# Kernel optimization log

Measured on AMD Instinct MI355X. Metric: run time of the kernel, lower is better.

The kernel has to match this reference:

```python
import jax, jax.numpy as jnp
import numpy as np

B, T, DIM = 2, 1024, 4096
H, Hk, D = 32, 8, 128
NREP = H // Hk
SCALE = 1.0 / np.sqrt(D)
LAMBDA_INIT = 0.8 - 0.6 * np.exp(-0.3 * 0)  # layer_idx=0 -> 0.2
EPS = 1e-6


def setup_inputs() -> dict:
    key = jax.random.key(0)
    ks = jax.random.split(key, 12)
    x = jax.random.normal(ks[0], (B, T, DIM), dtype=jnp.float32)
    cos = jax.random.uniform(ks[1], (T, D // 2), dtype=jnp.float32)
    sin = jax.random.uniform(ks[2], (T, D // 2), dtype=jnp.float32)
    wq = jax.random.normal(ks[3], (DIM, 2 * H * D), dtype=jnp.float32) * 0.02
    wk = jax.random.normal(ks[4], (DIM, 2 * Hk * D), dtype=jnp.float32) * 0.02
    wv = jax.random.normal(ks[5], (DIM, Hk * D), dtype=jnp.float32) * 0.02
    wo = jax.random.normal(ks[6], (H * D, DIM), dtype=jnp.float32) * 0.02
    lambda_q1 = jax.random.normal(ks[7], (H, D), dtype=jnp.float32) * 0.1
    lambda_k1 = jax.random.normal(ks[8], (H, D), dtype=jnp.float32) * 0.1
    lambda_q2 = jax.random.normal(ks[9], (H, D), dtype=jnp.float32) * 0.1
    lambda_k2 = jax.random.normal(ks[10], (H, D), dtype=jnp.float32) * 0.1
    subln_w = jnp.ones((D,), dtype=jnp.float32)
    return {"x": x, "cos": cos, "sin": sin, "wq": wq, "wk": wk, "wv": wv,
            "wo": wo, "lambda_q1": lambda_q1, "lambda_k1": lambda_k1,
            "lambda_q2": lambda_q2, "lambda_k2": lambda_k2, "subln_w": subln_w}


def _rope(xh, cos, sin):
    # xh: [B, h, T, D]; cos/sin: [T, D/2]
    x1, x2 = xh[..., : D // 2], xh[..., D // 2:]
    c = cos[None, None, :, :]
    s = sin[None, None, :, :]
    return jnp.concatenate([x1 * c - x2 * s, x2 * c + x1 * s], axis=-1)


def _causal_attn(q, k, v):
    # q,k,v: [B, H, T, D]
    s = jnp.einsum("bhqd,bhkd->bhqk", q, k) * SCALE
    causal = jnp.tril(jnp.ones((T, T), dtype=bool))
    s = jnp.where(causal[None, None], s, jnp.finfo(s.dtype).min)
    p = jax.nn.softmax(s, axis=-1)
    return jnp.einsum("bhqk,bhkd->bhqd", p, v)


def reference(x, cos, sin, wq, wk, wv, wo, lambda_q1, lambda_k1, lambda_q2, lambda_k2, subln_w):
    q_full = (x @ wq).reshape(B, T, 2 * H, D).transpose(0, 2, 1, 3)   # [B,2H,T,D]
    k_full = (x @ wk).reshape(B, T, 2 * Hk, D).transpose(0, 2, 1, 3)  # [B,2Hk,T,D]
    v = (x @ wv).reshape(B, T, Hk, D).transpose(0, 2, 1, 3)           # [B,Hk,T,D]

    q1, q2 = q_full[:, :H], q_full[:, H:]
    k1, k2 = k_full[:, :Hk], k_full[:, Hk:]

    q1 = _rope(q1, cos, sin)
    q2 = _rope(q2, cos, sin)
    k1 = _rope(k1, cos, sin)
    k2 = _rope(k2, cos, sin)

    def expand_kv(kv):  # [B,Hk,T,D] -> [B,H,T,D] (GQA repeat)
        return jnp.repeat(kv, NREP, axis=1)

    k1e, k2e, ve = expand_kv(k1), expand_kv(k2), expand_kv(v)

    a1 = _causal_attn(q1, k1e, ve)
    a2 = _causal_attn(q2, k2e, ve)

    lam = (jnp.exp(jnp.sum(lambda_q1 * lambda_k1, axis=-1))
           - jnp.exp(jnp.sum(lambda_q2 * lambda_k2, axis=-1))
           + LAMBDA_INIT)  # [H]
    diff = a1 - lam[None, :, None, None] * a2  # [B,H,T,D]

    # per-head-dim RMSNorm (subln)
    rms = jax.lax.rsqrt(jnp.mean(diff * diff, axis=-1, keepdims=True) + EPS)
    diff = diff * rms * subln_w

    out = diff.transpose(0, 2, 1, 3).reshape(B, T, H * D)
    return out @ wo
```

## Files before the change

kernel.cpp:

```cpp
#include <hip/hip_runtime.h>
#include <hip/hip_bf16.h>
#include <stdint.h>

typedef unsigned short u16;
typedef unsigned int u32;
typedef short bf16x8 __attribute__((ext_vector_type(8)));
typedef float f32x4 __attribute__((ext_vector_type(4)));

#define SCALE_F 0.088388347648318447f
#define LAMBDA_INIT_F 0.2f

__device__ __forceinline__ u16 f2bf(float f) {
  union { float f; u32 u; } v; v.f = f;
  u32 r = v.u + 0x7fffu + ((v.u >> 16) & 1u);
  return (u16)(r >> 16);
}
__device__ __forceinline__ float bf2f(u16 u) {
  union { u32 u; float f; } v; v.u = ((u32)u) << 16;
  return v.f;
}

typedef __attribute__((address_space(1))) void gvoid_t;
typedef __attribute__((address_space(3))) void lvoid_t;
__device__ __forceinline__ void gload16(const void* g, void* l) {
  __builtin_amdgcn_global_load_lds((gvoid_t*)g, (lvoid_t*)l, 16, 0, 0);
}

__global__ void cast_f32_bf16(const float4* __restrict__ in, uint2* __restrict__ out, int n4) {
  int i = blockIdx.x * 256 + threadIdx.x;
  if (i >= n4) return;
  float4 v = in[i];
  uint2 o;
  o.x = (u32)f2bf(v.x) | ((u32)f2bf(v.y) << 16);
  o.y = (u32)f2bf(v.z) | ((u32)f2bf(v.w) << 16);
  out[i] = o;
}

__global__ void trans_cast(const float* __restrict__ in, u16* __restrict__ out, int K, int N) {
  __shared__ float tile[64][33];
  int kt = blockIdx.y * 64, nt = blockIdx.x * 32;
  int x = threadIdx.x, y = threadIdx.y;
  #pragma unroll
  for (int j = 0; j < 8; ++j)
    tile[y + j * 8][x] = in[(size_t)(kt + y + j * 8) * N + nt + x];
  __syncthreads();
  #pragma unroll
  for (int j = 0; j < 4; ++j) {
    int n = y * 4 + j;
    u32 pk = (u32)f2bf(tile[2 * x][n]) | ((u32)f2bf(tile[2 * x + 1][n]) << 16);
    *(u32*)&out[(size_t)(nt + n) * K + kt + 2 * x] = pk;
  }
}

#define SQA(buf, t) { \
  gload16(Aq + (size_t)(t) * 32, (buf) + qdst); \
  gload16(Aq + (size_t)64 * K + (size_t)(t) * 32, (buf) + 2048 + qdst); }
#define SQB(buf, t) { \
  gload16(Bq + (size_t)(t) * 32, (buf) + qdst); \
  gload16(Bq + (size_t)64 * K + (size_t)(t) * 32, (buf) + 2048 + qdst); \
  gload16(Bq + (size_t)128 * K + (size_t)(t) * 32, (buf) + 4096 + qdst); \
  gload16(Bq + (size_t)192 * K + (size_t)(t) * 32, (buf) + 6144 + qdst); }
#define QMFMA16(O) { \
  acc[O+0][0] = __builtin_amdgcn_mfma_f32_16x16x32_bf16(a0, b0, acc[O+0][0], 0, 0, 0); \
  acc[O+0][1] = __builtin_amdgcn_mfma_f32_16x16x32_bf16(a0, b1, acc[O+0][1], 0, 0, 0); \
  acc[O+0][2] = __builtin_amdgcn_mfma_f32_16x16x32_bf16(a0, b2, acc[O+0][2], 0, 0, 0); \
  acc[O+0][3] = __builtin_amdgcn_mfma_f32_16x16x32_bf16(a0, b3, acc[O+0][3], 0, 0, 0); \
  acc[O+1][0] = __builtin_amdgcn_mfma_f32_16x16x32_bf16(a1, b0, acc[O+1][0], 0, 0, 0); \
  acc[O+1][1] = __builtin_amdgcn_mfma_f32_16x16x32_bf16(a1, b1, acc[O+1][1], 0, 0, 0); \
  acc[O+1][2] = __builtin_amdgcn_mfma_f32_16x16x32_bf16(a1, b2, acc[O+1][2], 0, 0, 0); \
  acc[O+1][3] = __builtin_amdgcn_mfma_f32_16x16x32_bf16(a1, b3, acc[O+1][3], 0, 0, 0); \
  acc[O+2][0] = __builtin_amdgcn_mfma_f32_16x16x32_bf16(a2, b0, acc[O+2][0], 0, 0, 0); \
  acc[O+2][1] = __builtin_amdgcn_mfma_f32_16x16x32_bf16(a2, b1, acc[O+2][1], 0, 0, 0); \
  acc[O+2][2] = __builtin_amdgcn_mfma_f32_16x16x32_bf16(a2, b2, acc[O+2][2], 0, 0, 0); \
  acc[O+2][3] = __builtin_amdgcn_mfma_f32_16x16x32_bf16(a2, b3, acc[O+2][3], 0, 0, 0); \
  acc[O+3][0] = __builtin_amdgcn_mfma_f32_16x16x32_bf16(a3, b0, acc[O+3][0], 0, 0, 0); \
  acc[O+3][1] = __builtin_amdgcn_mfma_f32_16x16x32_bf16(a3, b1, acc[O+3][1], 0, 0, 0); \
  acc[O+3][2] = __builtin_amdgcn_mfma_f32_16x16x32_bf16(a3, b2, acc[O+3][2], 0, 0, 0); \
  acc[O+3][3] = __builtin_amdgcn_mfma_f32_16x16x32_bf16(a3, b3, acc[O+3][3], 0, 0, 0); }

__global__ __launch_bounds__(256, 2) void gemmW(const u16* __restrict__ A,
                                                const u16* __restrict__ Bt,
                                                u16* __restrict__ C,
                                                int M, int N, int K, int TN) {
  extern __shared__ u16 lds[];
  const int tid = threadIdx.x;
  const int lane = tid & 63;
  const int wn = tid >> 6;
  const int ln = lane & 15, gr = lane >> 4;
  const int NT = K >> 5;

  const int bid = blockIdx.x;
  const int bn = (bid % TN) * 256;
  const int bm = (bid / TN) * 128;

  const int sch = (tid & 3) ^ ((tid >> 3) & 3);
  const u16* Aq = A + (size_t)(bm + (tid >> 2)) * K + sch * 8;
  const u16* Bq = Bt + (size_t)(bn + (tid >> 2)) * K + sch * 8;
  const int qdst = tid * 8;

  const int cfo = (gr ^ ((ln >> 1) & 3)) * 8;
  const int ab = ln * 32 + cfo;
  const int bb = wn * 2048 + ln * 32 + cfo;

  f32x4 acc[8][4] = {};
  bf16x8 a0, a1, a2, a3, b0, b1, b2, b3;

  SQA(lds, 0);
  SQB(lds + 12288, 0);
  SQA(lds + 4096, 1);
  SQB(lds + 20480, 1);
  asm volatile("s_waitcnt vmcnt(6)" ::: "memory");
  __builtin_amdgcn_s_barrier();

  int tm3 = 0;
  for (int t = 0; t < NT; ++t) {
    const u16* Ac = lds + tm3 * 4096;
    const u16* Bc = lds + 12288 + tm3 * 8192;
    int tn3 = tm3 + 2; if (tn3 >= 3) tn3 -= 3;
    u16* An = lds + tn3 * 4096;
    u16* Bn = lds + 12288 + tn3 * 8192;

    a0 = *(const bf16x8*)&Ac[ab];
    a1 = *(const bf16x8*)&Ac[ab + 512];
    a2 = *(const bf16x8*)&Ac[ab + 1024];
    a3 = *(const bf16x8*)&Ac[ab + 1536];
    b0 = *(const bf16x8*)&Bc[bb];
    b1 = *(const bf16x8*)&Bc[bb + 512];
    b2 = *(const bf16x8*)&Bc[bb + 1024];
    b3 = *(const bf16x8*)&Bc[bb + 1536];
    if (t + 2 < NT) SQA(An, t + 2);
    __builtin_amdgcn_s_barrier();
    __builtin_amdgcn_s_setprio(1);
    QMFMA16(0);
    __builtin_amdgcn_s_setprio(0);
    __builtin_amdgcn_s_barrier();

    a0 = *(const bf16x8*)&Ac[ab + 2048];
    a1 = *(const bf16x8*)&Ac[ab + 2560];
    a2 = *(const bf16x8*)&Ac[ab + 3072];
    a3 = *(const bf16x8*)&Ac[ab + 3584];
    if (t + 2 < NT) {
      SQB(Bn, t + 2);
      asm volatile("s_waitcnt vmcnt(6)" ::: "memory");
    } else {
      asm volatile("s_waitcnt vmcnt(0)" ::: "memory");
    }
    __builtin_amdgcn_s_barrier();
    __builtin_amdgcn_s_setprio(1);
    QMFMA16(4);
    __builtin_amdgcn_s_setprio(0);
    __builtin_amdgcn_s_barrier();

    tm3 = (tm3 + 1 == 3) ? 0 : tm3 + 1;
  }

  #pragma unroll
  for (int mf = 0; mf < 8; ++mf) {
    #pragma unroll
    for (int j = 0; j < 4; ++j) {
      int r = bm + mf * 16 + gr * 4 + j;
      #pragma unroll
      for (int nf = 0; nf < 4; ++nf) {
        int c = bn + wn * 64 + nf * 16 + ln;
        C[(size_t)r * N + c] = f2bf(acc[mf][nf][j]);
      }
    }
  }
}

#define STA(buf, t) { \
  gload16(Ab + (size_t)(t) * 64, (buf) + dsloc); \
  gload16(Ab + (size_t)32 * K + (size_t)(t) * 64, (buf) + 2048 + dsloc); \
  gload16(Ab + (size_t)64 * K + (size_t)(t) * 64, (buf) + 4096 + dsloc); \
  gload16(Ab + (size_t)96 * K + (size_t)(t) * 64, (buf) + 6144 + dsloc); }
#define STB(buf, t) { \
  gload16(Bb + (size_t)(t) * 64, (buf) + dsloc); \
  gload16(Bb + (size_t)32 * K + (size_t)(t) * 64, (buf) + 2048 + dsloc); \
  gload16(Bb + (size_t)64 * K + (size_t)(t) * 64, (buf) + 4096 + dsloc); \
  gload16(Bb + (size_t)96 * K + (size_t)(t) * 64, (buf) + 6144 + dsloc); }
#define MFMA16 { \
  acc[0][0] = __builtin_amdgcn_mfma_f32_16x16x32_bf16(a0, b0, acc[0][0], 0, 0, 0); \
  acc[0][1] = __builtin_amdgcn_mfma_f32_16x16x32_bf16(a0, b1, acc[0][1], 0, 0, 0); \
  acc[0][2] = __builtin_amdgcn_mfma_f32_16x16x32_bf16(a0, b2, acc[0][2], 0, 0, 0); \
  acc[0][3] = __builtin_amdgcn_mfma_f32_16x16x32_bf16(a0, b3, acc[0][3], 0, 0, 0); \
  acc[1][0] = __builtin_amdgcn_mfma_f32_16x16x32_bf16(a1, b0, acc[1][0], 0, 0, 0); \
  acc[1][1] = __builtin_amdgcn_mfma_f32_16x16x32_bf16(a1, b1, acc[1][1], 0, 0, 0); \
  acc[1][2] = __builtin_amdgcn_mfma_f32_16x16x32_bf16(a1, b2, acc[1][2], 0, 0, 0); \
  acc[1][3] = __builtin_amdgcn_mfma_f32_16x16x32_bf16(a1, b3, acc[1][3], 0, 0, 0); \
  acc[2][0] = __builtin_amdgcn_mfma_f32_16x16x32_bf16(a2, b0, acc[2][0], 0, 0, 0); \
  acc[2][1] = __builtin_amdgcn_mfma_f32_16x16x32_bf16(a2, b1, acc[2][1], 0, 0, 0); \
  acc[2][2] = __builtin_amdgcn_mfma_f32_16x16x32_bf16(a2, b2, acc[2][2], 0, 0, 0); \
  acc[2][3] = __builtin_amdgcn_mfma_f32_16x16x32_bf16(a2, b3, acc[2][3], 0, 0, 0); \
  acc[3][0] = __builtin_amdgcn_mfma_f32_16x16x32_bf16(a3, b0, acc[3][0], 0, 0, 0); \
  acc[3][1] = __builtin_amdgcn_mfma_f32_16x16x32_bf16(a3, b1, acc[3][1], 0, 0, 0); \
  acc[3][2] = __builtin_amdgcn_mfma_f32_16x16x32_bf16(a3, b2, acc[3][2], 0, 0, 0); \
  acc[3][3] = __builtin_amdgcn_mfma_f32_16x16x32_bf16(a3, b3, acc[3][3], 0, 0, 0); }

template <bool OUT_BF16>
__global__ __launch_bounds__(256, 2) void gemm8p(const u16* __restrict__ A,
                                                 const u16* __restrict__ Bt,
                                                 void* __restrict__ Cv,
                                                 int M, int N, int K, int TN) {
  extern __shared__ u16 lds[];
  const int tid = threadIdx.x;
  const int lane = tid & 63;
  const int wid = tid >> 6;
  const int wm = wid >> 1, wn = wid & 1;
  const int ln = lane & 15, gr = lane >> 4;
  const int NT = K >> 6;

  const int bid = blockIdx.x;
  const int bn = (bid % TN) * 128;
  const int bm = (bid / TN) * 128;

  const int srow = tid >> 3;
  const int sch = (tid & 7) ^ (srow & 7);
  const u16* Ab = A + (size_t)(bm + srow) * K + sch * 8;
  const u16* Bb = Bt + (size_t)(bn + srow) * K + sch * 8;
  const int dsloc = tid * 8;

  const int aro = (wm * 64 + ln) * 64;
  const int bro = (wn * 64 + ln) * 64;
  const int c0 = (gr ^ (ln & 7)) * 8;
  const int c1 = ((4 + gr) ^ (ln & 7)) * 8;

  f32x4 acc[4][4] = {};
  bf16x8 a0, a1, a2, a3, b0, b1, b2, b3;

  STA(lds, 0);
  STB(lds + 16384, 0);
  STB(lds + 24576, 1);
  asm volatile("s_waitcnt vmcnt(4)" ::: "memory");
  __builtin_amdgcn_s_barrier();

  int tm3 = 0;
  for (int t = 0; t < NT; ++t) {
    const u16* Ac = lds + (t & 1) * 8192;
    u16* An = lds + ((t + 1) & 1) * 8192;
    const u16* Bc = lds + 16384 + tm3 * 8192;
    int tn3 = tm3 + 2; if (tn3 >= 3) tn3 -= 3;
    u16* Bn = lds + 16384 + tn3 * 8192;

    a0 = *(const bf16x8*)&Ac[aro + c0];
    a1 = *(const bf16x8*)&Ac[aro + 1024 + c0];
    a2 = *(const bf16x8*)&Ac[aro + 2048 + c0];
    a3 = *(const bf16x8*)&Ac[aro + 3072 + c0];
    b0 = *(const bf16x8*)&Bc[bro + c0];
    b1 = *(const bf16x8*)&Bc[bro + 1024 + c0];
    b2 = *(const bf16x8*)&Bc[bro + 2048 + c0];
    b3 = *(const bf16x8*)&Bc[bro + 3072 + c0];
    if (t + 1 < NT) STA(An, t + 1);
    __builtin_amdgcn_s_barrier();
    __builtin_amdgcn_s_setprio(1);
    MFMA16;
    __builtin_amdgcn_s_setprio(0);
    __builtin_amdgcn_s_barrier();

    a0 = *(const bf16x8*)&Ac[aro + c1];
    a1 = *(const bf16x8*)&Ac[aro + 1024 + c1];
    a2 = *(const bf16x8*)&Ac[aro + 2048 + c1];
    a3 = *(const bf16x8*)&Ac[aro + 3072 + c1];
    b0 = *(const bf16x8*)&Bc[bro + c1];
    b1 = *(const bf16x8*)&Bc[bro + 1024 + c1];
    b2 = *(const bf16x8*)&Bc[bro + 2048 + c1];
    b3 = *(const bf16x8*)&Bc[bro + 3072 + c1];
    if (t + 2 < NT) {
      STB(Bn, t + 2);
      asm volatile("s_waitcnt vmcnt(4)" ::: "memory");
    } else {
      asm volatile("s_waitcnt vmcnt(0)" ::: "memory");
    }
    __builtin_amdgcn_s_barrier();
    __builtin_amdgcn_s_setprio(1);
    MFMA16;
    __builtin_amdgcn_s_setprio(0);
    __builtin_amdgcn_s_barrier();

    tm3 = (tm3 + 1 == 3) ? 0 : tm3 + 1;
  }

  #pragma unroll
  for (int mf = 0; mf < 4; ++mf) {
    #pragma unroll
    for (int j = 0; j < 4; ++j) {
      int r = bm + wm * 64 + mf * 16 + gr * 4 + j;
      #pragma unroll
      for (int nf = 0; nf < 4; ++nf) {
        int c = bn + wn * 64 + nf * 16 + ln;
        if (OUT_BF16) ((u16*)Cv)[(size_t)r * N + c] = f2bf(acc[mf][nf][j]);
        else          ((float*)Cv)[(size_t)r * N + c] = acc[mf][nf][j];
      }
    }
  }
}

__global__ void rope_kernel(const u16* __restrict__ in, u16* __restrict__ out,
                            const float* __restrict__ cosp, const float* __restrict__ sinp,
                            int NHh, int col_off) {
  int idx = blockIdx.x * 256 + threadIdx.x;
  int c = idx & 7;
  int t = (idx >> 3) & 1023;
  int h = (idx >> 13) % NHh;
  int b = (idx >> 13) / NHh;
  size_t src = (size_t)(b * 1024 + t) * 11264 + col_off + h * 128 + c * 8;
  bf16x8 v1 = *(const bf16x8*)&in[src];
  bf16x8 v2 = *(const bf16x8*)&in[src + 64];
  const float4* cp = (const float4*)&cosp[t * 64 + c * 8];
  const float4* sp = (const float4*)&sinp[t * 64 + c * 8];
  float4 c0 = cp[0], c1 = cp[1], s0 = sp[0], s1 = sp[1];
  float cc[8] = {c0.x, c0.y, c0.z, c0.w, c1.x, c1.y, c1.z, c1.w};
  float ss[8] = {s0.x, s0.y, s0.z, s0.w, s1.x, s1.y, s1.z, s1.w};
  bf16x8 o1, o2;
  #pragma unroll
  for (int e = 0; e < 8; ++e) {
    float x1 = bf2f((u16)v1[e]);
    float x2 = bf2f((u16)v2[e]);
    o1[e] = (short)f2bf(x1 * cc[e] - x2 * ss[e]);
    o2[e] = (short)f2bf(x2 * cc[e] + x1 * ss[e]);
  }
  size_t dst = ((size_t)(b * NHh + h) * 1024 + t) * 128 + c * 8;
  *(bf16x8*)&out[dst] = o1;
  *(bf16x8*)&out[dst + 64] = o2;
}

__global__ void vtrans_kernel(const u16* __restrict__ qkv, u16* __restrict__ vt) {
  __shared__ u16 tile[32][34];
  int bh = blockIdx.z;
  int t0 = blockIdx.x * 32, d0 = blockIdx.y * 32;
  int b = bh >> 3, hk = bh & 7;
  int x = threadIdx.x, y = threadIdx.y;
  #pragma unroll
  for (int j = 0; j < 32; j += 8)
    tile[y + j][x] = qkv[(size_t)(b * 1024 + t0 + y + j) * 11264 + 10240 + hk * 128 + d0 + x];
  __syncthreads();
  #pragma unroll
  for (int j = 0; j < 32; j += 8)
    vt[((size_t)bh * 128 + d0 + y + j) * 1024 + t0 + x] = tile[x][y + j];
}

__global__ void lam_kernel(const float* __restrict__ lq1, const float* __restrict__ lk1,
                           const float* __restrict__ lq2, const float* __restrict__ lk2,
                           float* __restrict__ lam) {
  int h = blockIdx.x, l = threadIdx.x;
  float p1 = lq1[h * 128 + l] * lk1[h * 128 + l] + lq1[h * 128 + 64 + l] * lk1[h * 128 + 64 + l];
  float p2 = lq2[h * 128 + l] * lk2[h * 128 + l] + lq2[h * 128 + 64 + l] * lk2[h * 128 + 64 + l];
  #pragma unroll
  for (int m = 32; m >= 1; m >>= 1) { p1 += __shfl_xor(p1, m); p2 += __shfl_xor(p2, m); }
  if (l == 0) lam[h] = expf(p1) - expf(p2) + LAMBDA_INIT_F;
}

__global__ __launch_bounds__(256) void attn_kernel(const u16* __restrict__ qr,
                                                   const u16* __restrict__ kr,
                                                   const u16* __restrict__ vt,
                                                   const float* __restrict__ lam,
                                                   const float* __restrict__ slw,
                                                   u16* __restrict__ attno) {
  __shared__ u16 k1s[32 * 136];
  __shared__ u16 k2s[32 * 136];
  __shared__ u16 vs[128 * 40];
  __shared__ u16 ps[4][2][640];
  const int qt = 15 - (int)blockIdx.x;
  const int h = blockIdx.y, b = blockIdx.z;
  const int tid = threadIdx.x, lane = tid & 63, w = tid >> 6;
  const int ln = lane & 15, gr = lane >> 4;
  const int hk = h >> 2;
  const int qrow0 = qt * 64 + w * 16;
  u16* psw1 = ps[w][0];
  u16* psw2 = ps[w][1];
  const float SL2E = 0.12751744006165926f;
  const float ML2E = 11.541560327111707f;

  bf16x8 q1f[4], q2f[4];
  {
    const u16* q1p = qr + ((size_t)(b * 64 + h) * 1024 + qrow0 + ln) * 128 + gr * 8;
    const u16* q2p = qr + ((size_t)(b * 64 + 32 + h) * 1024 + qrow0 + ln) * 128 + gr * 8;
    #pragma unroll
    for (int ds = 0; ds < 4; ++ds) {
      q1f[ds] = *(const bf16x8*)(q1p + ds * 32);
      q2f[ds] = *(const bf16x8*)(q2p + ds * 32);
    }
  }
  f32x4 acc1[8] = {}, acc2[8] = {};
  float l1[4] = {0.f, 0.f, 0.f, 0.f}, l2[4] = {0.f, 0.f, 0.f, 0.f};

  const u16* k1g = kr + (size_t)(b * 16 + hk) * 1024 * 128;
  const u16* k2g = kr + (size_t)(b * 16 + 8 + hk) * 1024 * 128;
  const u16* vg = vt + (size_t)(b * 8 + hk) * 128 * 1024;
  const int nkt = 2 * qt + 2;

  for (int kt = 0; kt < nkt; ++kt) {
    #pragma unroll
    for (int c = 0; c < 2; ++c) {
      int row = c * 16 + (tid >> 4);
      int ch = tid & 15;
      *(bf16x8*)&k1s[row * 136 + ch * 8] = *(const bf16x8*)&k1g[(size_t)(kt * 32 + row) * 128 + ch * 8];
      *(bf16x8*)&k2s[row * 136 + ch * 8] = *(const bf16x8*)&k2g[(size_t)(kt * 32 + row) * 128 + ch * 8];
      int dr = c * 64 + (tid >> 2);
      int ch2 = tid & 3;
      *(bf16x8*)&vs[dr * 40 + ch2 * 8] = *(const bf16x8*)&vg[(size_t)dr * 1024 + kt * 32 + ch2 * 8];
    }
    __syncthreads();

    f32x4 s1[2], s2[2];
    #pragma unroll
    for (int ct = 0; ct < 2; ++ct) {
      s1[ct] = (f32x4){0.f, 0.f, 0.f, 0.f};
      s2[ct] = (f32x4){0.f, 0.f, 0.f, 0.f};
      #pragma unroll
      for (int ds = 0; ds < 4; ++ds) {
        bf16x8 kf1 = *(const bf16x8*)&k1s[(ct * 16 + ln) * 136 + ds * 32 + gr * 8];
        s1[ct] = __builtin_amdgcn_mfma_f32_16x16x32_bf16(q1f[ds], kf1, s1[ct], 0, 0, 0);
        bf16x8 kf2 = *(const bf16x8*)&k2s[(ct * 16 + ln) * 136 + ds * 32 + gr * 8];
        s2[ct] = __builtin_amdgcn_mfma_f32_16x16x32_bf16(q2f[ds], kf2, s2[ct], 0, 0, 0);
      }
    }
    #pragma unroll
    for (int j = 0; j < 4; ++j) {
      int row = qrow0 + gr * 4 + j;
      bool msk0 = (kt * 32 + ln) > row;
      bool msk1 = (kt * 32 + 16 + ln) > row;
      float t10 = msk0 ? -1e30f : fmaf(s1[0][j], SL2E, -ML2E);
      float t11 = msk1 ? -1e30f : fmaf(s1[1][j], SL2E, -ML2E);
      float t20 = msk0 ? -1e30f : fmaf(s2[0][j], SL2E, -ML2E);
      float t21 = msk1 ? -1e30f : fmaf(s2[1][j], SL2E, -ML2E);
      u16 b10 = f2bf(exp2f(t10)), b11 = f2bf(exp2f(t11));
      u16 b20 = f2bf(exp2f(t20)), b21 = f2bf(exp2f(t21));
      int ro = (gr * 4 + j) * 40;
      psw1[ro + ln] = b10; psw1[ro + 16 + ln] = b11;
      psw2[ro + ln] = b20; psw2[ro + 16 + ln] = b21;
      l1[j] += bf2f(b10) + bf2f(b11);
      l2[j] += bf2f(b20) + bf2f(b21);
    }
    bf16x8 pf1 = *(const bf16x8*)&psw1[ln * 40 + gr * 8];
    bf16x8 pf2 = *(const bf16x8*)&psw2[ln * 40 + gr * 8];
    #pragma unroll
    for (int dt = 0; dt < 8; ++dt) {
      bf16x8 vf = *(const bf16x8*)&vs[(dt * 16 + ln) * 40 + gr * 8];
      acc1[dt] = __builtin_amdgcn_mfma_f32_16x16x32_bf16(pf1, vf, acc1[dt], 0, 0, 0);
      acc2[dt] = __builtin_amdgcn_mfma_f32_16x16x32_bf16(pf2, vf, acc2[dt], 0, 0, 0);
    }
    __syncthreads();
  }

  float inv1[4], inv2[4];
  #pragma unroll
  for (int j = 0; j < 4; ++j) {
    float a = l1[j], c = l2[j];
    a += __shfl_xor(a, 1); a += __shfl_xor(a, 2); a += __shfl_xor(a, 4); a += __shfl_xor(a, 8);
    c += __shfl_xor(c, 1); c += __shfl_xor(c, 2); c += __shfl_xor(c, 4); c += __shfl_xor(c, 8);
    inv1[j] = 1.f / a;
    inv2[j] = 1.f / c;
  }

  float lamv = lam[h];
  float ssq[4] = {0.f, 0.f, 0.f, 0.f};
  #pragma unroll
  for (int dt = 0; dt < 8; ++dt)
    #pragma unroll
    for (int j = 0; j < 4; ++j) {
      float d = acc1[dt][j] * inv1[j] - lamv * (acc2[dt][j] * inv2[j]);
      acc1[dt][j] = d;
      ssq[j] += d * d;
    }
  #pragma unroll
  for (int j = 0; j < 4; ++j) {
    float s = ssq[j];
    s += __shfl_xor(s, 1);
    s += __shfl_xor(s, 2);
    s += __shfl_xor(s, 4);
    s += __shfl_xor(s, 8);
    ssq[j] = rsqrtf(s * (1.0f / 128.0f) + 1e-6f);
  }
  #pragma unroll
  for (int dt = 0; dt < 8; ++dt) {
    float wgt = slw[dt * 16 + ln];
    #pragma unroll
    for (int j = 0; j < 4; ++j) {
      int row = qrow0 + gr * 4 + j;
      attno[(size_t)(b * 1024 + row) * 4096 + h * 128 + dt * 16 + ln] = f2bf(acc1[dt][j] * ssq[j] * wgt);
    }
  }
}

extern "C" void kernel_launch(void* const* d_in, const int* in_sizes, int n_in,
                              void* d_out, int out_size, void* d_ws, size_t ws_size,
                              hipStream_t stream) {
  (void)in_sizes; (void)n_in; (void)out_size; (void)ws_size;
  const float* x    = (const float*)d_in[0];
  const float* cosp = (const float*)d_in[1];
  const float* sinp = (const float*)d_in[2];
  const float* wq   = (const float*)d_in[3];
  const float* wk   = (const float*)d_in[4];
  const float* wv   = (const float*)d_in[5];
  const float* wo   = (const float*)d_in[6];
  const float* lq1  = (const float*)d_in[7];
  const float* lk1  = (const float*)d_in[8];
  const float* lq2  = (const float*)d_in[9];
  const float* lk2  = (const float*)d_in[10];
  const float* slw  = (const float*)d_in[11];
  float* out = (float*)d_out;
  char* ws = (char*)d_ws;

  u16* xb    = (u16*)(ws);
  u16* wqkvt = (u16*)(ws + 16777216);
  u16* qr    = (u16*)(ws + 16777216);
  u16* kr    = (u16*)(ws + 50331648);
  u16* vtp   = (u16*)(ws + 58720256);
  u16* attno = (u16*)(ws + 62914560);
  u16* qkv   = (u16*)(ws + 109051904);
  u16* wot   = (u16*)(ws + 109051904);
  float* lam = (float*)(ws + 155189248);

  cast_f32_bf16<<<8192, 256, 0, stream>>>((const float4*)x, (uint2*)xb, 2097152);
  trans_cast<<<dim3(256, 64), dim3(32, 8), 0, stream>>>(wq, wqkvt, 4096, 8192);
  trans_cast<<<dim3(64, 64),  dim3(32, 8), 0, stream>>>(wk, wqkvt + (size_t)8192 * 4096, 4096, 2048);
  trans_cast<<<dim3(32, 64),  dim3(32, 8), 0, stream>>>(wv, wqkvt + (size_t)10240 * 4096, 4096, 1024);
  gemmW<<<704, 256, 73728, stream>>>(xb, wqkvt, qkv, 2048, 11264, 4096, 44);
  rope_kernel<<<4096, 256, 0, stream>>>(qkv, qr, cosp, sinp, 64, 0);
  rope_kernel<<<1024, 256, 0, stream>>>(qkv, kr, cosp, sinp, 16, 8192);
  vtrans_kernel<<<dim3(32, 4, 16), dim3(32, 8), 0, stream>>>(qkv, vtp);
  trans_cast<<<dim3(128, 64), dim3(32, 8), 0, stream>>>(wo, wot, 4096, 4096);
  lam_kernel<<<32, 64, 0, stream>>>(lq1, lk1, lq2, lk2, lam);
  attn_kernel<<<dim3(16, 32, 2), 256, 0, stream>>>(qr, kr, vtp, lam, slw, attno);
  gemm8p<false><<<512, 256, 81920, stream>>>(attno, wot, (void*)out, 2048, 4096, 4096, 32);
}
```

Before: 484.5 us.

## Double-buffer K/V tiles in attention and use 128-row query blocks

Result: faster. 431.6 us (-10.9%).

```diff
diff --git a/kernel.cpp b/kernel.cpp
--- a/kernel.cpp
+++ b/kernel.cpp
@@ -349,22 +349,22 @@
   if (l == 0) lam[h] = expf(p1) - expf(p2) + LAMBDA_INIT_F;
 }
 
-__global__ __launch_bounds__(256) void attn_kernel(const u16* __restrict__ qr,
+__global__ __launch_bounds__(512) void attn_kernel(const u16* __restrict__ qr,
                                                    const u16* __restrict__ kr,
                                                    const u16* __restrict__ vt,
                                                    const float* __restrict__ lam,
                                                    const float* __restrict__ slw,
                                                    u16* __restrict__ attno) {
-  __shared__ u16 k1s[32 * 136];
-  __shared__ u16 k2s[32 * 136];
-  __shared__ u16 vs[128 * 40];
-  __shared__ u16 ps[4][2][640];
-  const int qt = 15 - (int)blockIdx.x;
-  const int h = blockIdx.y, b = blockIdx.z;
+  __shared__ u16 k1s[2][32 * 136];
+  __shared__ u16 k2s[2][32 * 136];
+  __shared__ u16 vs[2][128 * 40];
+  __shared__ u16 ps[8][2][640];
+  const int bx = blockIdx.x, h = blockIdx.y, b = blockIdx.z;
+  const int qt = (b == 0) ? (7 - bx) : bx;
   const int tid = threadIdx.x, lane = tid & 63, w = tid >> 6;
   const int ln = lane & 15, gr = lane >> 4;
   const int hk = h >> 2;
-  const int qrow0 = qt * 64 + w * 16;
+  const int qrow0 = qt * 128 + w * 16;
   u16* psw1 = ps[w][0];
   u16* psw2 = ps[w][1];
   const float SL2E = 0.12751744006165926f;
@@ -386,20 +386,31 @@
   const u16* k1g = kr + (size_t)(b * 16 + hk) * 1024 * 128;
   const u16* k2g = kr + (size_t)(b * 16 + 8 + hk) * 1024 * 128;
   const u16* vg = vt + (size_t)(b * 8 + hk) * 128 * 1024;
-  const int nkt = 2 * qt + 2;
-
+  const int nkt = 4 * qt + 4;
+
+  const int krow = tid >> 4, kch = tid & 15;
+  const int vdr = tid >> 2, vch = tid & 3;
+  const u16* k1p = k1g + (size_t)krow * 128 + kch * 8;
+  const u16* k2p = k2g + (size_t)krow * 128 + kch * 8;
+  const u16* vp = vg + (size_t)vdr * 1024 + vch * 8;
+  const int kdst = krow * 136 + kch * 8;
+  const int vdst = vdr * 40 + vch * 8;
+
+  bf16x8 r0 = *(const bf16x8*)(k1p);
+  bf16x8 r1 = *(const bf16x8*)(k2p);
+  bf16x8 r2 = *(const bf16x8*)(vp);
+  *(bf16x8*)&k1s[0][kdst] = r0;
+  *(bf16x8*)&k2s[0][kdst] = r1;
+  *(bf16x8*)&vs[0][vdst] = r2;
+  __syncthreads();
+
+  int cur = 0;
   for (int kt = 0; kt < nkt; ++kt) {
-    #pragma unroll
-    for (int c = 0; c < 2; ++c) {
-      int row = c * 16 + (tid >> 4);
-      int ch = tid & 15;
-      *(bf16x8*)&k1s[row * 136 + ch * 8] = *(const bf16x8*)&k1g[(size_t)(kt * 32 + row) * 128 + ch * 8];
-      *(bf16x8*)&k2s[row * 136 + ch * 8] = *(const bf16x8*)&k2g[(size_t)(kt * 32 + row) * 128 + ch * 8];
-      int dr = c * 64 + (tid >> 2);
-      int ch2 = tid & 3;
-      *(bf16x8*)&vs[dr * 40 + ch2 * 8] = *(const bf16x8*)&vg[(size_t)dr * 1024 + kt * 32 + ch2 * 8];
-    }
-    __syncthreads();
+    if (kt + 1 < nkt) {
+      r0 = *(const bf16x8*)(k1p + (size_t)(kt + 1) * 4096);
+      r1 = *(const bf16x8*)(k2p + (size_t)(kt + 1) * 4096);
+      r2 = *(const bf16x8*)(vp + (size_t)(kt + 1) * 32);
+    }
 
     f32x4 s1[2], s2[2];
     #pragma unroll
@@ -408,9 +419,9 @@
       s2[ct] = (f32x4){0.f, 0.f, 0.f, 0.f};
       #pragma unroll
       for (int ds = 0; ds < 4; ++ds) {
-        bf16x8 kf1 = *(const bf16x8*)&k1s[(ct * 16 + ln) * 136 + ds * 32 + gr * 8];
+        bf16x8 kf1 = *(const bf16x8*)&k1s[cur][(ct * 16 + ln) * 136 + ds * 32 + gr * 8];
         s1[ct] = __builtin_amdgcn_mfma_f32_16x16x32_bf16(q1f[ds], kf1, s1[ct], 0, 0, 0);
-        bf16x8 kf2 = *(const bf16x8*)&k2s[(ct * 16 + ln) * 136 + ds * 32 + gr * 8];
+        bf16x8 kf2 = *(const bf16x8*)&k2s[cur][(ct * 16 + ln) * 136 + ds * 32 + gr * 8];
         s2[ct] = __builtin_amdgcn_mfma_f32_16x16x32_bf16(q2f[ds], kf2, s2[ct], 0, 0, 0);
       }
     }
@@ -435,11 +446,18 @@
     bf16x8 pf2 = *(const bf16x8*)&psw2[ln * 40 + gr * 8];
     #pragma unroll
     for (int dt = 0; dt < 8; ++dt) {
-      bf16x8 vf = *(const bf16x8*)&vs[(dt * 16 + ln) * 40 + gr * 8];
+      bf16x8 vf = *(const bf16x8*)&vs[cur][(dt * 16 + ln) * 40 + gr * 8];
       acc1[dt] = __builtin_amdgcn_mfma_f32_16x16x32_bf16(pf1, vf, acc1[dt], 0, 0, 0);
       acc2[dt] = __builtin_amdgcn_mfma_f32_16x16x32_bf16(pf2, vf, acc2[dt], 0, 0, 0);
     }
+
+    if (kt + 1 < nkt) {
+      *(bf16x8*)&k1s[cur ^ 1][kdst] = r0;
+      *(bf16x8*)&k2s[cur ^ 1][kdst] = r1;
+      *(bf16x8*)&vs[cur ^ 1][vdst] = r2;
+    }
     __syncthreads();
+    cur ^= 1;
   }
 
   float inv1[4], inv2[4];
@@ -521,6 +539,6 @@
   vtrans_kernel<<<dim3(32, 4, 16), dim3(32, 8), 0, stream>>>(qkv, vtp);
   trans_cast<<<dim3(128, 64), dim3(32, 8), 0, stream>>>(wo, wot, 4096, 4096);
   lam_kernel<<<32, 64, 0, stream>>>(lq1, lk1, lq2, lk2, lam);
-  attn_kernel<<<dim3(16, 32, 2), 256, 0, stream>>>(qr, kr, vtp, lam, slw, attno);
+  attn_kernel<<<dim3(8, 32, 2), 512, 0, stream>>>(qr, kr, vtp, lam, slw, attno);
   gemm8p<false><<<512, 256, 81920, stream>>>(attno, wot, (void*)out, 2048, 4096, 4096, 32);
 }
```
